# Kernel tuning notes

Measured on AMD Instinct MI355X. Metric: run time of the kernel, lower is better.

Reference implementation:

```python
import jax, jax.numpy as jnp
import numpy as np
import math

L, D, NH, HD, H, V = 6, 384, 6, 64, 768, 4096
B, T = 4, 2048


def setup_inputs() -> dict:
    key = jax.random.key(0)
    ks = jax.random.split(key, 16)
    s = 0.02
    inp = {
        "x": jax.random.randint(ks[0], (B, T), 0, V, dtype=jnp.int32),
        "emb": jax.random.normal(ks[1], (V, D), jnp.float32) * s,
        "wq": jax.random.normal(ks[2], (L, D, D), jnp.float32) * s,
        "wk": jax.random.normal(ks[3], (L, D, D), jnp.float32) * s,
        "wv": jax.random.normal(ks[4], (L, D, D), jnp.float32) * s,
        "wo": jax.random.normal(ks[5], (L, D, D), jnp.float32) * s,
        "ln1": jnp.ones((L, D), jnp.float32),
        "ln2": jnp.ones((L, D), jnp.float32),
        "w1": jax.random.normal(ks[6], (L, D, H), jnp.float32) * s,
        "b1": jnp.zeros((L, H), jnp.float32),
        "w2": jax.random.normal(ks[7], (L, H, D), jnp.float32) * s,
        "b2": jnp.zeros((L, D), jnp.float32),
        "lnf": jnp.ones((D,), jnp.float32),
        "head": jax.random.normal(ks[8], (D, V), jnp.float32) * s,
    }
    return inp


def _rms(x, w):
    return x * jax.lax.rsqrt(jnp.mean(x * x, axis=-1, keepdims=True) + 1e-6) * w


def _attn(x, wq, wk, wv, wo):
    b, t, _ = x.shape
    q = (x @ wq).reshape(b, t, NH, HD).transpose(0, 2, 1, 3)  # [b,h,t,hd]
    k = (x @ wk).reshape(b, t, NH, HD).transpose(0, 2, 1, 3)
    v = (x @ wv).reshape(b, t, NH, HD).transpose(0, 2, 1, 3)
    scores = jnp.einsum('bhqd,bhkd->bhqk', q, k) / math.sqrt(HD)
    causal = jnp.tril(jnp.ones((t, t), bool))
    scores = jnp.where(causal, scores, -jnp.inf)
    a = jax.nn.softmax(scores, axis=-1)
    o = jnp.einsum('bhqk,bhkd->bhqd', a, v)
    o = o.transpose(0, 2, 1, 3).reshape(b, t, D)
    return o @ wo


def reference(x, emb, wq, wk, wv, wo, ln1, ln2, w1, b1, w2, b2, lnf, head):
    h = emb[x]  # [B,T,D]
    mid = None
    for i in range(L):
        h = h + _attn(_rms(h, ln1[i]), wq[i], wk[i], wv[i], wo[i])
        hn = _rms(h, ln2[i])
        ff = jax.nn.gelu(hn @ w1[i] + b1[i], approximate=False) @ w2[i] + b2[i]
        h = h + ff
        if i == 2:
            mid = h
    logits = _rms(h, lnf) @ head
    return logits, mid
```

## Files before the change

kernel.cpp:

```cpp
#include <hip/hip_runtime.h>
#include <hip/hip_bf16.h>
#include <math.h>

#define L_  6
#define D_  384
#define NH_ 6
#define HD_ 64
#define HF_ 768
#define V_  4096
#define B_  4
#define T_  2048
#define BT_ (B_*T_)

typedef unsigned short u16;
typedef __attribute__((ext_vector_type(8))) short short8;
typedef __attribute__((ext_vector_type(4))) float f32x4;

__device__ __forceinline__ float bf2f(u16 u){
  union { unsigned int i; float f; } c; c.i = ((unsigned int)u)<<16; return c.f;
}
__device__ __forceinline__ u16 f2bf(float f){
  union { float f; unsigned int i; } c; c.f = f;
  unsigned int x = c.i;
  x += 0x7fffu + ((x>>16)&1u);
  return (u16)(x>>16);
}
__device__ __forceinline__ f32x4 mfma16(short8 a, short8 b, f32x4 c){
  return __builtin_amdgcn_mfma_f32_16x16x32_bf16(a,b,c,0,0,0);
}
template<int CTRL>
__device__ __forceinline__ float dppmax(float x){
  int v = __builtin_amdgcn_update_dpp(0, __builtin_bit_cast(int, x), CTRL, 0xf, 0xf, true);
  return fmaxf(x, __builtin_bit_cast(float, v));
}
__device__ __forceinline__ float rowmax16(float x){
  x = dppmax<0xB1>(x);
  x = dppmax<0x4E>(x);
  x = dppmax<0x141>(x);
  x = dppmax<0x140>(x);
  return x;
}
#define GLD16(gp, lp) __builtin_amdgcn_global_load_lds( \
    (const __attribute__((address_space(1))) void*)(gp), \
    (__attribute__((address_space(3))) void*)(lp), 16, 0, 0)

__global__ void embed_kernel(const int* __restrict__ x, const float* __restrict__ emb,
                             float* __restrict__ h){
  const int idx = blockIdx.x*256 + threadIdx.x;
  if(idx >= BT_*D_) return;
  const int t = idx / D_;
  const int d = idx - t*D_;
  h[idx] = emb[(size_t)x[t]*D_ + d];
}

__global__ __launch_bounds__(256) void wtrans_kernel(const float* __restrict__ src,
    u16* __restrict__ dst, int K, int N, size_t srcBatch, size_t dstBatch){
  __shared__ float tile[32][33];
  src += (size_t)blockIdx.z*srcBatch;
  dst += (size_t)blockIdx.z*dstBatch;
  const int tx = threadIdx.x&31, ty = threadIdx.x>>5;
  const int n0 = blockIdx.x*32, k0 = blockIdx.y*32;
  #pragma unroll
  for(int j=0;j<4;j++)
    tile[ty+j*8][tx] = src[(size_t)(k0+ty+j*8)*N + n0+tx];
  __syncthreads();
  #pragma unroll
  for(int j=0;j<4;j++)
    dst[(size_t)(n0+ty+j*8)*K + k0+tx] = f2bf(tile[tx][ty+j*8]);
}

__global__ __launch_bounds__(256) void rms_kernel(const float* __restrict__ h,
                                                  const float* __restrict__ w,
                                                  u16* __restrict__ out){
  const int wave = threadIdx.x>>6, lane = threadIdx.x&63;
  const size_t row = (size_t)blockIdx.x*4 + wave;
  const float* hr = h + row*D_;
  float v[6]; float ss = 0.f;
  #pragma unroll
  for(int i=0;i<6;i++){ v[i] = hr[lane + i*64]; ss += v[i]*v[i]; }
  #pragma unroll
  for(int o=1;o<64;o<<=1) ss += __shfl_xor(ss, o);
  const float rn = rsqrtf(ss*(1.f/D_) + 1e-6f);
  u16* orow = out + row*D_;
  #pragma unroll
  for(int i=0;i<6;i++) orow[lane+i*64] = f2bf(v[i]*rn*w[lane+i*64]);
}

template<int MODE, int K, int BM, int BN>
__global__ __launch_bounds__(256) void gemm_kernel(
    const u16* __restrict__ A, const u16* __restrict__ Wt, int N,
    const float* __restrict__ bias, u16* __restrict__ out, float* __restrict__ fout,
    u16* __restrict__ qo, u16* __restrict__ ko, u16* __restrict__ vo,
    float* __restrict__ fout2)
{
  __shared__ u16 As[2][BM*64];
  __shared__ u16 Bs[2][BN*64];
  constexpr int WM  = (BM==128) ? ((BN==128)?2:4) : ((BN==128)?1:2);
  constexpr int WN  = 4/WM;
  constexpr int MI  = (BM/WM)/16;
  constexpr int NI  = (BN/WN)/16;
  constexpr int NKT = K/64;
  constexpr int APW = (BM/8)/4;
  constexpr int BPW = (BN/8)/4;
  constexpr int VM  = APW + BPW;

  const int w = threadIdx.x>>6, lane = threadIdx.x&63;
  const int l16 = lane&15, quad = lane>>4;
  const int r0 = blockIdx.y*BM, n0 = blockIdx.x*BN;
  const int mst = lane>>3;
  const int cst = (lane&7) ^ (lane>>3);

  const int wrow = (w%WM)*(BM/WM);
  const int wcol = (w/WM)*(BN/WN);

  f32x4 acc[MI][NI];
  #pragma unroll
  for(int mi=0;mi<MI;mi++)
    #pragma unroll
    for(int ni=0;ni<NI;ni++){ acc[mi][ni][0]=0.f; acc[mi][ni][1]=0.f; acc[mi][ni][2]=0.f; acc[mi][ni][3]=0.f; }

  auto stage = [&](int kt, int bu){
    const int k0 = kt*64;
    #pragma unroll
    for(int i=0;i<APW;i++){
      const int j = w*APW+i;
      GLD16(A + (size_t)(r0+j*8+mst)*K + k0 + cst*8, &As[bu][j*512]);
    }
    #pragma unroll
    for(int i=0;i<BPW;i++){
      const int j = w*BPW+i;
      GLD16(Wt + (size_t)(n0+j*8+mst)*K + k0 + cst*8, &Bs[bu][j*512]);
    }
  };

  stage(0, 0);
  for(int kt=0; kt<NKT; kt++){
    const u16* Ac = As[kt&1];
    const u16* Bc = Bs[kt&1];
    if(kt+1 < NKT){
      stage(kt+1, (kt+1)&1);
      if constexpr(VM==8)      asm volatile("s_waitcnt vmcnt(8)" ::: "memory");
      else if constexpr(VM==6) asm volatile("s_waitcnt vmcnt(6)" ::: "memory");
      else                     asm volatile("s_waitcnt vmcnt(4)" ::: "memory");
    } else {
      asm volatile("s_waitcnt vmcnt(0)" ::: "memory");
    }
    __builtin_amdgcn_s_barrier();
    asm volatile("" ::: "memory");

    __builtin_amdgcn_s_setprio(1);
    #pragma unroll
    for(int ks=0;ks<2;ks++){
      short8 av[MI], bv[NI];
      #pragma unroll
      for(int mi=0;mi<MI;mi++){
        const int m = wrow + mi*16 + l16;
        av[mi] = *(const short8*)&Ac[m*64 + (((ks*4+quad)^(l16&7))*8)];
      }
      #pragma unroll
      for(int ni=0;ni<NI;ni++){
        const int n = wcol + ni*16 + l16;
        bv[ni] = *(const short8*)&Bc[n*64 + (((ks*4+quad)^(l16&7))*8)];
      }
      #pragma unroll
      for(int mi=0;mi<MI;mi++)
        #pragma unroll
        for(int ni=0;ni<NI;ni++)
          acc[mi][ni] = mfma16(av[mi], bv[ni], acc[mi][ni]);
    }
    __builtin_amdgcn_s_setprio(0);
    if(kt+1 < NKT){
      asm volatile("" ::: "memory");
      __builtin_amdgcn_s_barrier();
    }
  }

  #pragma unroll
  for(int mi=0;mi<MI;mi++){
    #pragma unroll
    for(int ni=0;ni<NI;ni++){
      const int col = n0 + wcol + ni*16 + l16;
      #pragma unroll
      for(int r=0;r<4;r++){
        const int row = r0 + wrow + mi*16 + quad*4 + r;
        float v = acc[mi][ni][r];
        if(MODE==0){
          fout[(size_t)row*N + col] = v;
        } else if(MODE==1){
          v += bias[col];
          v = 0.5f*v*(1.f + erff(v*0.70710678118f));
          out[(size_t)row*N + col] = f2bf(v);
        } else if(MODE==2){
          if(bias) v += bias[col];
          fout[(size_t)row*N + col] += v;
        } else if(MODE==4){
          v += bias[col];
          const float nv = fout[(size_t)row*N + col] + v;
          fout[(size_t)row*N + col] = nv;
          fout2[(size_t)row*N + col] = nv;
        } else {
          if(col < D_)        qo[(size_t)row*D_ + col]      = f2bf(v);
          else if(col < 2*D_) ko[(size_t)row*D_ + (col-D_)] = f2bf(v);
          else {
            const int cv = col - 2*D_;
            const int hh = cv>>6, dd = cv&63;
            const int bb = row>>11, tt = row&(T_-1);
            vo[(((size_t)(bb*NH_+hh))*HD_ + dd)*T_ + tt] = f2bf(v);
          }
        }
      }
    }
  }
}

__global__ __launch_bounds__(256) void flash_kernel(const u16* __restrict__ q,
    const u16* __restrict__ k, const u16* __restrict__ vt, u16* __restrict__ ao){
  __shared__ u16 Ks[2][64*64];
  __shared__ u16 Vs[2][80*64];
  __shared__ __align__(16) u16 Pb[4][16*64];
  const int tid = threadIdx.x;
  const int w = tid>>6, lane = tid&63;
  const int l16 = lane&15, quad = lane>>4;
  const int bh = blockIdx.y, b = bh/NH_, h = bh - b*NH_;
  const int qt = (gridDim.x-1) - blockIdx.x;
  const int qw = qt*64 + w*16;

  {
    const int idx0 = tid*8;
    #pragma unroll
    for(int i=0;i<8;i++){
      const int idx = idx0 + i;
      const int bu = idx>>10, rem = idx&1023;
      Vs[bu][(64 + (rem>>6))*64 + (rem&63)] = ((rem>>6)==0) ? (u16)0x3F80 : (u16)0;
    }
  }
  __syncthreads();

  const u16* qp = q + ((size_t)(b*T_ + qw + l16))*D_ + h*HD_ + quad*8;
  short8 qf0 = *(const short8*)(qp);
  short8 qf1 = *(const short8*)(qp + 32);

  const u16* kbase = k + (size_t)(b*T_)*D_ + h*HD_;
  const u16* vbase = vt + (size_t)(b*NH_ + h)*HD_*T_;
  u16* Pw = &Pb[w][0];

  const int srow = lane>>3;
  const int schunk = lane&7;
  const int kgc = schunk ^ srow;

  float m[4];
  f32x4 o[5];
  #pragma unroll
  for(int r=0;r<4;r++) m[r] = -1e30f;
  #pragma unroll
  for(int c=0;c<5;c++){ o[c][0]=0.f; o[c][1]=0.f; o[c][2]=0.f; o[c][3]=0.f; }

  const int nkt = qt + 1;

  #pragma unroll
  for(int i=0;i<2;i++){
    const int j = w*2+i;
    GLD16(kbase + (size_t)(j*8 + srow)*D_ + kgc*8, &Ks[0][j*512]);
  }
  #pragma unroll
  for(int i=0;i<2;i++){
    const int j = w*2+i;
    GLD16(vbase + (size_t)(j*8 + srow)*T_ + (schunk^srow)*8, &Vs[0][j*512]);
  }

  for(int kt=0; kt<nkt; kt++){
    const u16* Kc = Ks[kt&1];
    const u16* Vc = Vs[kt&1];
    if(kt+1 < nkt){
      const int kb2 = (kt+1)*64;
      #pragma unroll
      for(int i=0;i<2;i++){
        const int j = w*2+i;
        GLD16(kbase + (size_t)(kb2 + j*8 + srow)*D_ + kgc*8, &Ks[(kt+1)&1][j*512]);
      }
      #pragma unroll
      for(int i=0;i<2;i++){
        const int j = w*2+i;
        GLD16(vbase + (size_t)(j*8 + srow)*T_ + kb2 + (schunk^srow)*8, &Vs[(kt+1)&1][j*512]);
      }
      asm volatile("s_waitcnt vmcnt(4)" ::: "memory");
    } else {
      asm volatile("s_waitcnt vmcnt(0)" ::: "memory");
    }
    __builtin_amdgcn_s_barrier();

    float s[4][4];
    __builtin_amdgcn_s_setprio(1);
    #pragma unroll
    for(int c=0;c<4;c++){
      const int krow = c*16 + l16;
      short8 kf0 = *(const short8*)&Kc[krow*64 + ((quad^(l16&7))*8)];
      short8 kf1 = *(const short8*)&Kc[krow*64 + (((4+quad)^(l16&7))*8)];
      f32x4 sa = {0.f,0.f,0.f,0.f};
      sa = mfma16(qf0, kf0, sa);
      sa = mfma16(qf1, kf1, sa);
      #pragma unroll
      for(int r=0;r<4;r++) s[c][r] = sa[r]*0.125f;
    }
    __builtin_amdgcn_s_setprio(0);
    if(kt == nkt-1){
      const int kb = kt*64;
      #pragma unroll
      for(int c=0;c<4;c++){
        const int kpos = kb + c*16 + l16;
        #pragma unroll
        for(int r=0;r<4;r++)
          if(kpos > qw + quad*4 + r) s[c][r] = -1e30f;
      }
    }
    float tmr[4];
    #pragma unroll
    for(int r=0;r<4;r++){
      float tm = fmaxf(fmaxf(s[0][r], s[1][r]), fmaxf(s[2][r], s[3][r]));
      tmr[r] = rowmax16(tm);
    }
    float need = tmr[0] - m[0];
    #pragma unroll
    for(int r=1;r<4;r++) need = fmaxf(need, tmr[r] - m[r]);
    if(!__all(need <= 8.f)){
      #pragma unroll
      for(int r=0;r<4;r++){
        const float mn = fmaxf(m[r], tmr[r]);
        const float al = __expf(m[r] - mn);
        #pragma unroll
        for(int c=0;c<5;c++) o[c][r] *= al;
        m[r] = mn;
      }
    }
    #pragma unroll
    for(int r=0;r<4;r++){
      const int prow = quad*4 + r;
      #pragma unroll
      for(int c=0;c<4;c++){
        const float p = __expf(s[c][r] - m[r]);
        Pw[prow*64 + (((c*2 + (l16>>3)) ^ (prow&7))<<3) + (l16&7)] = f2bf(p);
      }
    }
    __builtin_amdgcn_s_setprio(1);
    #pragma unroll
    for(int kk=0;kk<2;kk++){
      short8 pf = *(const short8*)&Pw[l16*64 + (((kk*4+quad) ^ (l16&7))<<3)];
      #pragma unroll
      for(int c=0;c<5;c++){
        const int dd = c*16 + l16;
        short8 vf = *(const short8*)&Vc[dd*64 + (((kk*4+quad)^(l16&7))<<3)];
        o[c] = mfma16(pf, vf, o[c]);
      }
    }
    __builtin_amdgcn_s_setprio(0);
    __builtin_amdgcn_s_barrier();
  }
  #pragma unroll
  for(int r=0;r<4;r++){
    const float lr = __shfl(o[4][r], quad<<4, 64);
    const float il = 1.f / lr;
    const size_t row = (size_t)(b*T_ + qw + quad*4 + r);
    #pragma unroll
    for(int c=0;c<4;c++)
      ao[row*D_ + h*HD_ + c*16 + l16] = f2bf(o[c][r] * il);
  }
}

extern "C" void kernel_launch(void* const* d_in, const int* in_sizes, int n_in,
                              void* d_out, int out_size, void* d_ws, size_t ws_size,
                              hipStream_t stream) {
  const int*   x    = (const int*)d_in[0];
  const float* emb  = (const float*)d_in[1];
  const float* wq   = (const float*)d_in[2];
  const float* wk   = (const float*)d_in[3];
  const float* wv   = (const float*)d_in[4];
  const float* wo   = (const float*)d_in[5];
  const float* ln1  = (const float*)d_in[6];
  const float* ln2  = (const float*)d_in[7];
  const float* w1   = (const float*)d_in[8];
  const float* b1   = (const float*)d_in[9];
  const float* w2   = (const float*)d_in[10];
  const float* b2   = (const float*)d_in[11];
  const float* lnf  = (const float*)d_in[12];
  const float* head = (const float*)d_in[13];
  float* out = (float*)d_out;

  char* ws = (char*)d_ws; size_t off = 0;
  auto alloc = [&](size_t bytes)->void* {
    void* p = ws + off; off += (bytes + 255) & ~(size_t)255; return p;
  };
  float* hbuf  = (float*)alloc((size_t)BT_*D_*4);
  u16* xn    = (u16*)alloc((size_t)BT_*D_*2);
  u16* qb    = (u16*)alloc((size_t)BT_*D_*2);
  u16* kb    = (u16*)alloc((size_t)BT_*D_*2);
  u16* vtb   = (u16*)alloc((size_t)BT_*D_*2);
  u16* aob   = (u16*)alloc((size_t)BT_*D_*2);
  u16* midb  = (u16*)alloc((size_t)BT_*HF_*2);
  u16* qkvt  = (u16*)alloc((size_t)L_*3*D_*D_*2);
  u16* wot   = (u16*)alloc((size_t)L_*D_*D_*2);
  u16* w1t   = (u16*)alloc((size_t)L_*HF_*D_*2);
  u16* w2t   = (u16*)alloc((size_t)L_*D_*HF_*2);
  u16* headt = (u16*)alloc((size_t)V_*D_*2);

  const dim3 blk(256);
  wtrans_kernel<<<dim3(D_/32, D_/32, L_), blk, 0, stream>>>(wq, qkvt,           D_, D_, (size_t)D_*D_, (size_t)3*D_*D_);
  wtrans_kernel<<<dim3(D_/32, D_/32, L_), blk, 0, stream>>>(wk, qkvt + D_*D_,   D_, D_, (size_t)D_*D_, (size_t)3*D_*D_);
  wtrans_kernel<<<dim3(D_/32, D_/32, L_), blk, 0, stream>>>(wv, qkvt + 2*D_*D_, D_, D_, (size_t)D_*D_, (size_t)3*D_*D_);
  wtrans_kernel<<<dim3(D_/32, D_/32, L_), blk, 0, stream>>>(wo, wot,            D_, D_, (size_t)D_*D_, (size_t)D_*D_);
  wtrans_kernel<<<dim3(HF_/32, D_/32, L_), blk, 0, stream>>>(w1, w1t, D_, HF_, (size_t)D_*HF_, (size_t)HF_*D_);
  wtrans_kernel<<<dim3(D_/32, HF_/32, L_), blk, 0, stream>>>(w2, w2t, HF_, D_, (size_t)D_*HF_, (size_t)D_*HF_);
  wtrans_kernel<<<dim3(V_/32, D_/32, 1),  blk, 0, stream>>>(head, headt, D_, V_, 0, 0);

  embed_kernel<<<(BT_*D_ + 255)/256, blk, 0, stream>>>(x, emb, hbuf);

  for(int li=0; li<L_; li++){
    rms_kernel<<<BT_/4, blk, 0, stream>>>(hbuf, ln1 + li*D_, xn);
    gemm_kernel<3,D_,64,128><<<dim3(3*D_/128, BT_/64), blk, 0, stream>>>(
        xn, qkvt + (size_t)li*3*D_*D_, 3*D_, nullptr, nullptr, nullptr, qb, kb, vtb, nullptr);
    flash_kernel<<<dim3(T_/64, B_*NH_), blk, 0, stream>>>(qb, kb, vtb, aob);
    gemm_kernel<2,D_,64,64><<<dim3(D_/64, BT_/64), blk, 0, stream>>>(
        aob, wot + (size_t)li*D_*D_, D_, nullptr, nullptr, hbuf, nullptr, nullptr, nullptr, nullptr);
    rms_kernel<<<BT_/4, blk, 0, stream>>>(hbuf, ln2 + li*D_, xn);
    gemm_kernel<1,D_,64,128><<<dim3(HF_/128, BT_/64), blk, 0, stream>>>(
        xn, w1t + (size_t)li*HF_*D_, HF_, b1 + li*HF_, midb, nullptr, nullptr, nullptr, nullptr, nullptr);
    if(li == 2)
      gemm_kernel<4,HF_,64,64><<<dim3(D_/64, BT_/64), blk, 0, stream>>>(
          midb, w2t + (size_t)li*D_*HF_, D_, b2 + li*D_, nullptr, hbuf, nullptr, nullptr, nullptr,
          out + (size_t)BT_*V_);
    else
      gemm_kernel<2,HF_,64,64><<<dim3(D_/64, BT_/64), blk, 0, stream>>>(
          midb, w2t + (size_t)li*D_*HF_, D_, b2 + li*D_, nullptr, hbuf, nullptr, nullptr, nullptr, nullptr);
  }
  rms_kernel<<<BT_/4, blk, 0, stream>>>(hbuf, lnf, xn);
  gemm_kernel<0,D_,64,128><<<dim3(V_/128, BT_/64), blk, 0, stream>>>(
      xn, headt, V_, nullptr, nullptr, out, nullptr, nullptr, nullptr, nullptr);
}
```

Measured before the change: 1.113 ms.

## Keep flash-attention P in registers via transposed MFMA and permlane swaps

The QK^T MFMA operands are swapped so each lane holds one query row's scores. This makes the row max a per-lane reduction instead of DPP cross-lane ops, and the softmax scale is folded into an exp2 constant using raw v_exp_f32. P is packed to bf16 with v_cvt_pk_bf16_f32 and rearranged with permlane32/16 swaps straight into the PV MFMA operand, which removes the LDS round trip for P. The output is staged through the reused K buffer so it can be written with 16-byte vector stores. The lazy rescale threshold is raised, and this relies on gfx950-specific instructions and careful lane layouts.

```diff
diff --git a/kernel.cpp b/kernel.cpp
--- a/kernel.cpp
+++ b/kernel.cpp
@@ -15,6 +15,7 @@
 typedef unsigned short u16;
 typedef __attribute__((ext_vector_type(8))) short short8;
 typedef __attribute__((ext_vector_type(4))) float f32x4;
+typedef __attribute__((ext_vector_type(4))) int   int4v;
 
 __device__ __forceinline__ float bf2f(u16 u){
   union { unsigned int i; float f; } c; c.i = ((unsigned int)u)<<16; return c.f;
@@ -28,17 +29,17 @@
 __device__ __forceinline__ f32x4 mfma16(short8 a, short8 b, f32x4 c){
   return __builtin_amdgcn_mfma_f32_16x16x32_bf16(a,b,c,0,0,0);
 }
-template<int CTRL>
-__device__ __forceinline__ float dppmax(float x){
-  int v = __builtin_amdgcn_update_dpp(0, __builtin_bit_cast(int, x), CTRL, 0xf, 0xf, true);
-  return fmaxf(x, __builtin_bit_cast(float, v));
-}
-__device__ __forceinline__ float rowmax16(float x){
-  x = dppmax<0xB1>(x);
-  x = dppmax<0x4E>(x);
-  x = dppmax<0x141>(x);
-  x = dppmax<0x140>(x);
-  return x;
+__device__ __forceinline__ float exp2a(float x){
+  float r; asm("v_exp_f32 %0, %1" : "=v"(r) : "v"(x)); return r;
+}
+__device__ __forceinline__ int cvtpkbf(float lo, float hi){
+  int r; asm("v_cvt_pk_bf16_f32 %0, %1, %2" : "=v"(r) : "v"(lo), "v"(hi)); return r;
+}
+__device__ __forceinline__ void pl32(int &a, int &b){
+  asm("v_permlane32_swap_b32 %0, %1" : "+v"(a), "+v"(b));
+}
+__device__ __forceinline__ void pl16(int &a, int &b){
+  asm("v_permlane16_swap_b32 %0, %1" : "+v"(a), "+v"(b));
 }
 #define GLD16(gp, lp) __builtin_amdgcn_global_load_lds( \
     (const __attribute__((address_space(1))) void*)(gp), \
@@ -217,10 +218,10 @@
     const u16* __restrict__ k, const u16* __restrict__ vt, u16* __restrict__ ao){
   __shared__ u16 Ks[2][64*64];
   __shared__ u16 Vs[2][80*64];
-  __shared__ __align__(16) u16 Pb[4][16*64];
   const int tid = threadIdx.x;
   const int w = tid>>6, lane = tid&63;
   const int l16 = lane&15, quad = lane>>4;
+  const bool hi32 = lane >= 32;
   const int bh = blockIdx.y, b = bh/NH_, h = bh - b*NH_;
   const int qt = (gridDim.x-1) - blockIdx.x;
   const int qw = qt*64 + w*16;
@@ -242,16 +243,14 @@
 
   const u16* kbase = k + (size_t)(b*T_)*D_ + h*HD_;
   const u16* vbase = vt + (size_t)(b*NH_ + h)*HD_*T_;
-  u16* Pw = &Pb[w][0];
 
   const int srow = lane>>3;
   const int schunk = lane&7;
   const int kgc = schunk ^ srow;
 
-  float m[4];
+  const float sc2 = 0.18033688011112042f;
+  float m2 = -1e30f;
   f32x4 o[5];
-  #pragma unroll
-  for(int r=0;r<4;r++) m[r] = -1e30f;
   #pragma unroll
   for(int c=0;c<5;c++){ o[c][0]=0.f; o[c][1]=0.f; o[c][2]=0.f; o[c][3]=0.f; }
 
@@ -297,73 +296,87 @@
       short8 kf0 = *(const short8*)&Kc[krow*64 + ((quad^(l16&7))*8)];
       short8 kf1 = *(const short8*)&Kc[krow*64 + (((4+quad)^(l16&7))*8)];
       f32x4 sa = {0.f,0.f,0.f,0.f};
-      sa = mfma16(qf0, kf0, sa);
-      sa = mfma16(qf1, kf1, sa);
-      #pragma unroll
-      for(int r=0;r<4;r++) s[c][r] = sa[r]*0.125f;
+      sa = mfma16(kf0, qf0, sa);
+      sa = mfma16(kf1, qf1, sa);
+      #pragma unroll
+      for(int r=0;r<4;r++) s[c][r] = sa[r]*sc2;
     }
     __builtin_amdgcn_s_setprio(0);
     if(kt == nkt-1){
       const int kb = kt*64;
       #pragma unroll
-      for(int c=0;c<4;c++){
-        const int kpos = kb + c*16 + l16;
+      for(int c=0;c<4;c++)
         #pragma unroll
-        for(int r=0;r<4;r++)
-          if(kpos > qw + quad*4 + r) s[c][r] = -1e30f;
-      }
-    }
-    float tmr[4];
-    #pragma unroll
-    for(int r=0;r<4;r++){
-      float tm = fmaxf(fmaxf(s[0][r], s[1][r]), fmaxf(s[2][r], s[3][r]));
-      tmr[r] = rowmax16(tm);
-    }
-    float need = tmr[0] - m[0];
-    #pragma unroll
-    for(int r=1;r<4;r++) need = fmaxf(need, tmr[r] - m[r]);
-    if(!__all(need <= 8.f)){
-      #pragma unroll
-      for(int r=0;r<4;r++){
-        const float mn = fmaxf(m[r], tmr[r]);
-        const float al = __expf(m[r] - mn);
+        for(int r=0;r<4;r++){
+          const int kpos = kb + c*16 + quad*4 + r;
+          if(kpos > qw + l16) s[c][r] = -1e30f;
+        }
+    }
+    float tm = s[0][0];
+    #pragma unroll
+    for(int c=0;c<4;c++)
+      #pragma unroll
+      for(int r=0;r<4;r++) tm = fmaxf(tm, s[c][r]);
+    if(!__all(tm - m2 <= 11.5f)){
+      float t = fmaxf(tm, __shfl_xor(tm, 16));
+      t = fmaxf(t, __shfl_xor(t, 32));
+      const float mn = fmaxf(m2, t);
+      const float al = exp2a(m2 - mn);
+      #pragma unroll
+      for(int c=0;c<5;c++)
         #pragma unroll
-        for(int c=0;c<5;c++) o[c][r] *= al;
-        m[r] = mn;
-      }
-    }
-    #pragma unroll
-    for(int r=0;r<4;r++){
-      const int prow = quad*4 + r;
-      #pragma unroll
-      for(int c=0;c<4;c++){
-        const float p = __expf(s[c][r] - m[r]);
-        Pw[prow*64 + (((c*2 + (l16>>3)) ^ (prow&7))<<3) + (l16&7)] = f2bf(p);
-      }
+        for(int r=0;r<4;r++) o[c][r] *= al;
+      m2 = mn;
+    }
+    int P01[4], P23[4];
+    #pragma unroll
+    for(int c=0;c<4;c++){
+      const float p0 = exp2a(s[c][0] - m2);
+      const float p1 = exp2a(s[c][1] - m2);
+      const float p2 = exp2a(s[c][2] - m2);
+      const float p3 = exp2a(s[c][3] - m2);
+      P01[c] = cvtpkbf(p0, p1);
+      P23[c] = cvtpkbf(p2, p3);
     }
     __builtin_amdgcn_s_setprio(1);
     #pragma unroll
     for(int kk=0;kk<2;kk++){
-      short8 pf = *(const short8*)&Pw[l16*64 + (((kk*4+quad) ^ (l16&7))<<3)];
-      #pragma unroll
-      for(int c=0;c<5;c++){
-        const int dd = c*16 + l16;
+      int xA = P01[kk*2],   xB = xA; pl32(xA,xB); pl16(xA,xB);
+      int yA = P01[kk*2+1], yB = yA; pl32(yA,yB); pl16(yA,yB);
+      int zA = P23[kk*2],   zB = zA; pl32(zA,zB); pl16(zA,zB);
+      int wA = P23[kk*2+1], wB = wA; pl32(wA,wB); pl16(wA,wB);
+      int4v bi;
+      bi.x = hi32 ? yA : xA;
+      bi.y = hi32 ? wA : zA;
+      bi.z = hi32 ? yB : xB;
+      bi.w = hi32 ? wB : zB;
+      const short8 pb = __builtin_bit_cast(short8, bi);
+      #pragma unroll
+      for(int c2=0;c2<5;c2++){
+        const int dd = c2*16 + l16;
         short8 vf = *(const short8*)&Vc[dd*64 + (((kk*4+quad)^(l16&7))<<3)];
-        o[c] = mfma16(pf, vf, o[c]);
+        o[c2] = mfma16(vf, pb, o[c2]);
       }
     }
     __builtin_amdgcn_s_setprio(0);
     __builtin_amdgcn_s_barrier();
   }
-  #pragma unroll
-  for(int r=0;r<4;r++){
-    const float lr = __shfl(o[4][r], quad<<4, 64);
-    const float il = 1.f / lr;
-    const size_t row = (size_t)(b*T_ + qw + quad*4 + r);
-    #pragma unroll
-    for(int c=0;c<4;c++)
-      ao[row*D_ + h*HD_ + c*16 + l16] = f2bf(o[c][r] * il);
-  }
+
+  const float sum = __shfl(o[4][0], l16, 64);
+  const float il = 1.f / sum;
+  u16* Tb = &Ks[0][0] + w*1152;
+  #pragma unroll
+  for(int c2=0;c2<4;c2++){
+    const int d01 = cvtpkbf(o[c2][0]*il, o[c2][1]*il);
+    const int d23 = cvtpkbf(o[c2][2]*il, o[c2][3]*il);
+    *(int*)&Tb[l16*72 + c2*16 + quad*4]     = d01;
+    *(int*)&Tb[l16*72 + c2*16 + quad*4 + 2] = d23;
+  }
+  const short8 r0 = *(const short8*)&Tb[l16*72 + quad*8];
+  const short8 r1 = *(const short8*)&Tb[l16*72 + (quad+4)*8];
+  u16* aop = ao + (size_t)(b*T_ + qw + l16)*D_ + h*HD_;
+  *(short8*)&aop[quad*8]     = r0;
+  *(short8*)&aop[(quad+4)*8] = r1;
 }
 
 extern "C" void kernel_launch(void* const* d_in, const int* in_sizes, int n_in,
```

Measured after the change: 1.042 ms. -6.4%, faster.
